# Kernel optimization log

Hardware: AMD Instinct MI355X
Metric: run time of the kernel (lower is better)

The kernel has to match this reference:

```python
import jax, jax.numpy as jnp
import numpy as np

N = 5000
E = 160000
H = 6   # num_heads
D = 64  # out feats per head
IN = 131


def _gat_layer(h, W, al, ar, b, src, dst, activate):
    """DGL-style GATConv: fc -> edge attention -> edge softmax -> scatter sum."""
    n = h.shape[0]
    f = (h @ W).reshape(n, H, D)                      # [N,H,D]
    el = (f * al).sum(-1)                             # [N,H]
    er = (f * ar).sum(-1)                             # [N,H]
    e = jax.nn.leaky_relu(el[src] + er[dst], 0.2)     # [E,H]
    emax = jax.ops.segment_max(e, dst, num_segments=n)
    ex = jnp.exp(e - emax[dst])
    den = jax.ops.segment_sum(ex, dst, num_segments=n)
    alpha = ex / den[dst]                             # [E,H] edge softmax per dst
    out = jax.ops.segment_sum(f[src] * alpha[:, :, None], dst, num_segments=n)
    out = out + b.reshape(H, D)
    return jax.nn.elu(out) if activate else out


def setup_inputs() -> dict:
    ks = jax.random.split(jax.random.key(0), 24)
    s = 0.05
    inp = {
        "nfeats": jax.random.normal(ks[0], (N, IN), jnp.float32),
        "dis": jax.random.uniform(ks[1], (N, N), jnp.float32),
        "src": jax.random.randint(ks[2], (E,), 0, N),
        "dst": jax.random.randint(ks[3], (E,), 0, N),
    }
    dims_in = [IN, H * D, H * D, H * D]
    for l in range(4):
        inp[f"w{l}"] = jax.random.normal(ks[4 + 4 * l], (dims_in[l], H * D), jnp.float32) * s
        inp[f"al{l}"] = jax.random.normal(ks[5 + 4 * l], (H, D), jnp.float32) * s
        inp[f"ar{l}"] = jax.random.normal(ks[6 + 4 * l], (H, D), jnp.float32) * s
        inp[f"b{l}"] = jax.random.normal(ks[7 + 4 * l], (H * D,), jnp.float32) * s
    inp["pw"] = jax.random.normal(ks[20], (129,), jnp.float32) * s
    inp["pb"] = jax.random.normal(ks[21], (), jnp.float32) * s
    return inp


def reference(nfeats, dis, src, dst,
              w0, al0, ar0, b0, w1, al1, ar1, b1,
              w2, al2, ar2, b2, w3, al3, ar3, b3, pw, pb):
    n = nfeats.shape[0]
    h = nfeats
    h = _gat_layer(h, w0, al0, ar0, b0, src, dst, True).reshape(n, H * D)
    h = _gat_layer(h, w1, al1, ar1, b1, src, dst, True).reshape(n, H * D)
    h = _gat_layer(h, w2, al2, ar2, b2, src, dst, True).reshape(n, H * D)
    emb = _gat_layer(h, w3, al3, ar3, b3, src, dst, False).mean(axis=1)  # [N,64]
    # pair_emb[i,j] = [emb[j], emb[i], dis[i,j]] -> Linear(129,1) -> tanh
    s1 = emb @ pw[:D]        # coefficient on emb[j]
    s2 = emb @ pw[D:2 * D]   # coefficient on emb[i]
    OD = jnp.tanh(s2[:, None] + s1[None, :] + dis * pw[2 * D] + pb)
    return OD
```

## Files before the change

kernel.cpp:

```cpp
#include <hip/hip_runtime.h>
#include <math.h>

#define N_NODES 5000
#define E_EDGES 160000
#define H_HEADS 6
#define D_FEAT  64
#define IN_FEAT 131
#define HD      384
#define NC4     (N_NODES/4)
#define AGG_CAP 1024
#define MPAD    5024
#define KP0     160

typedef float vf4   __attribute__((ext_vector_type(4)));
typedef float f32x4 __attribute__((ext_vector_type(4)));
typedef _Float16 h16;
typedef _Float16 half8 __attribute__((ext_vector_type(8)));

__global__ void k_count(const int* __restrict__ dst, int* __restrict__ deg) {
    int e = blockIdx.x * blockDim.x + threadIdx.x;
    if (e < E_EDGES) atomicAdd(&deg[dst[e]], 1);
}

__global__ void k_scan(int* __restrict__ deg, int* __restrict__ row_ptr) {
    __shared__ int part[1024];
    const int T = 1024;
    int t = threadIdx.x;
    const int per = (N_NODES + T - 1) / T;
    int start = t * per;
    int s = 0;
    for (int i = 0; i < per; i++) {
        int idx = start + i;
        if (idx < N_NODES) s += deg[idx];
    }
    part[t] = s;
    __syncthreads();
    for (int off = 1; off < T; off <<= 1) {
        int v = (t >= off) ? part[t - off] : 0;
        __syncthreads();
        part[t] += v;
        __syncthreads();
    }
    int excl = (t == 0) ? 0 : part[t - 1];
    for (int i = 0; i < per; i++) {
        int idx = start + i;
        if (idx < N_NODES) {
            row_ptr[idx] = excl;
            excl += deg[idx];
            deg[idx] = 0;
        }
    }
    if (t == T - 1) row_ptr[N_NODES] = part[T - 1];
}

__global__ void k_fill(const int* __restrict__ src, const int* __restrict__ dst,
                       const int* __restrict__ row_ptr,
                       int* __restrict__ cursor, int* __restrict__ csrc) {
    int e = blockIdx.x * blockDim.x + threadIdx.x;
    if (e < E_EDGES) {
        int d = dst[e];
        int p = atomicAdd(&cursor[d], 1);
        csrc[row_ptr[d] + p] = src[e];
    }
}

__global__ void k_cvt_a0(const float* __restrict__ A, h16* __restrict__ hi,
                         h16* __restrict__ lo) {
    int idx = blockIdx.x * blockDim.x + threadIdx.x;
    if (idx >= MPAD * KP0) return;
    int r = idx / KP0, k = idx - r * KP0;
    float v = (r < N_NODES && k < IN_FEAT) ? A[r * IN_FEAT + k] : 0.f;
    h16 h = (h16)v;
    hi[idx] = h;
    lo[idx] = (h16)(v - (float)h);
}

__global__ void k_cvt_w(const float* __restrict__ W, h16* __restrict__ hi,
                        h16* __restrict__ lo, int K, int KP) {
    int idx = blockIdx.x * blockDim.x + threadIdx.x;
    if (idx >= HD * KP) return;
    int n = idx / KP, k = idx - n * KP;
    float v = (k < K) ? W[(size_t)k * HD + n] : 0.f;
    h16 h = (h16)v;
    hi[idx] = h;
    lo[idx] = (h16)(v - (float)h);
}

__global__ __launch_bounds__(64, 2) void k_gemm_mfma(
        const h16* __restrict__ Ahi, const h16* __restrict__ Alo,
        const h16* __restrict__ Wthi, const h16* __restrict__ Wtlo,
        const float* __restrict__ al, const float* __restrict__ ar,
        float* __restrict__ C, float* __restrict__ el, float* __restrict__ er,
        int KP) {
    int lane = threadIdx.x;
    int h = blockIdx.x;
    int rb = blockIdx.y * 32;
    int cb = h * 64;
    int l15 = lane & 15, lg = lane >> 4;
    f32x4 acc[2][4] = {};

    const h16* a0h = Ahi + (size_t)(rb + l15) * KP + (lg << 3);
    const h16* a0l = Alo + (size_t)(rb + l15) * KP + (lg << 3);
    const h16* a1h = a0h + (size_t)16 * KP;
    const h16* a1l = a0l + (size_t)16 * KP;
    const h16* bh = Wthi + (size_t)(cb + l15) * KP + (lg << 3);
    const h16* bl = Wtlo + (size_t)(cb + l15) * KP + (lg << 3);

#pragma unroll 2
    for (int k0 = 0; k0 < KP; k0 += 32) {
        half8 A0h = *(const half8*)(a0h + k0);
        half8 A0l = *(const half8*)(a0l + k0);
        half8 A1h = *(const half8*)(a1h + k0);
        half8 A1l = *(const half8*)(a1l + k0);
#pragma unroll
        for (int t = 0; t < 4; t++) {
            half8 Bh = *(const half8*)(bh + (size_t)t * 16 * KP + k0);
            half8 Bl = *(const half8*)(bl + (size_t)t * 16 * KP + k0);
            acc[0][t] = __builtin_amdgcn_mfma_f32_16x16x32_f16(A0h, Bh, acc[0][t], 0, 0, 0);
            acc[0][t] = __builtin_amdgcn_mfma_f32_16x16x32_f16(A0l, Bh, acc[0][t], 0, 0, 0);
            acc[0][t] = __builtin_amdgcn_mfma_f32_16x16x32_f16(A0h, Bl, acc[0][t], 0, 0, 0);
            acc[1][t] = __builtin_amdgcn_mfma_f32_16x16x32_f16(A1h, Bh, acc[1][t], 0, 0, 0);
            acc[1][t] = __builtin_amdgcn_mfma_f32_16x16x32_f16(A1l, Bh, acc[1][t], 0, 0, 0);
            acc[1][t] = __builtin_amdgcn_mfma_f32_16x16x32_f16(A1h, Bl, acc[1][t], 0, 0, 0);
        }
    }

    float alv[4], arv[4];
#pragma unroll
    for (int t = 0; t < 4; t++) {
        alv[t] = al[h * D_FEAT + t * 16 + l15];
        arv[t] = ar[h * D_FEAT + t * 16 + l15];
    }
#pragma unroll
    for (int m = 0; m < 2; m++) {
#pragma unroll
        for (int r = 0; r < 4; r++) {
            int grow = rb + m * 16 + lg * 4 + r;
            float sl = 0.f, sr = 0.f;
#pragma unroll
            for (int t = 0; t < 4; t++) {
                float v = acc[m][t][r];
                if (grow < N_NODES) C[(size_t)grow * HD + cb + t * 16 + l15] = v;
                sl += v * alv[t];
                sr += v * arv[t];
            }
#pragma unroll
            for (int off = 1; off < 16; off <<= 1) {
                sl += __shfl_xor(sl, off);
                sr += __shfl_xor(sr, off);
            }
            if (l15 == 0 && grow < N_NODES) {
                el[grow * H_HEADS + h] = sl;
                er[grow * H_HEADS + h] = sr;
            }
        }
    }
}

__global__ __launch_bounds__(384) void k_agg(const float* __restrict__ f,
                                             const float* __restrict__ el,
                                             const float* __restrict__ er,
                                             const float* __restrict__ bias,
                                             const int* __restrict__ row_ptr,
                                             const int* __restrict__ csrc,
                                             float* __restrict__ out, int activate,
                                             h16* __restrict__ nhi,
                                             h16* __restrict__ nlo) {
    __shared__ int   s_src[AGG_CAP];
    __shared__ float s_x[H_HEADS][AGG_CAP];
    __shared__ float sh_inv[H_HEADS];
    int node = blockIdx.x;
    int t = threadIdx.x;
    int h = t >> 6, lane = t & 63;
    int r0 = row_ptr[node], r1 = row_ptr[node + 1];
    int deg = r1 - r0;
    int dcap = deg < AGG_CAP ? deg : AGG_CAP;
    float er_h = er[node * H_HEADS + h];

    for (int i = t; i < dcap; i += 384) s_src[i] = csrc[r0 + i];
    __syncthreads();

    float m = -1e30f;
    for (int i = lane; i < dcap; i += 64) {
        int s = s_src[i];
        float x = el[s * H_HEADS + h] + er_h;
        x = x >= 0.f ? x : 0.2f * x;
        s_x[h][i] = x;
        m = fmaxf(m, x);
    }
    for (int i = AGG_CAP + lane; i < deg; i += 64) {
        int s = csrc[r0 + i];
        float x = el[s * H_HEADS + h] + er_h;
        x = x >= 0.f ? x : 0.2f * x;
        m = fmaxf(m, x);
    }
    for (int off = 32; off; off >>= 1) m = fmaxf(m, __shfl_down(m, off));
    m = __shfl(m, 0);

    float ssum = 0.f;
    for (int i = lane; i < dcap; i += 64) {
        float w = __expf(s_x[h][i] - m);
        s_x[h][i] = w;
        ssum += w;
    }
    for (int i = AGG_CAP + lane; i < deg; i += 64) {
        int s = csrc[r0 + i];
        float x = el[s * H_HEADS + h] + er_h;
        x = x >= 0.f ? x : 0.2f * x;
        ssum += __expf(x - m);
    }
    for (int off = 32; off; off >>= 1) ssum += __shfl_down(ssum, off);
    if (lane == 0) sh_inv[h] = (ssum > 0.f) ? 1.f / ssum : 0.f;
    __syncthreads();
    float inv = sh_inv[h];

    const float* fh = f + h * D_FEAT + lane;
    float acc = 0.f;
    int i = 0;
    int lim = dcap & ~7;
    for (; i < lim; i += 8) {
        int s0 = s_src[i + 0], s1 = s_src[i + 1], s2 = s_src[i + 2], s3 = s_src[i + 3];
        int s4 = s_src[i + 4], s5 = s_src[i + 5], s6 = s_src[i + 6], s7 = s_src[i + 7];
        float f0 = fh[(size_t)s0 * HD], f1 = fh[(size_t)s1 * HD];
        float f2 = fh[(size_t)s2 * HD], f3 = fh[(size_t)s3 * HD];
        float f4 = fh[(size_t)s4 * HD], f5 = fh[(size_t)s5 * HD];
        float f6 = fh[(size_t)s6 * HD], f7 = fh[(size_t)s7 * HD];
        acc += s_x[h][i + 0] * f0;
        acc += s_x[h][i + 1] * f1;
        acc += s_x[h][i + 2] * f2;
        acc += s_x[h][i + 3] * f3;
        acc += s_x[h][i + 4] * f4;
        acc += s_x[h][i + 5] * f5;
        acc += s_x[h][i + 6] * f6;
        acc += s_x[h][i + 7] * f7;
    }
    for (; i < dcap; i++) {
        acc += s_x[h][i] * fh[(size_t)s_src[i] * HD];
    }
    for (i = AGG_CAP; i < deg; i++) {
        int s = csrc[r0 + i];
        float x = el[s * H_HEADS + h] + er_h;
        x = x >= 0.f ? x : 0.2f * x;
        acc += __expf(x - m) * fh[(size_t)s * HD];
    }
    float o = acc * inv + bias[h * D_FEAT + lane];
    if (activate) o = o > 0.f ? o : (__expf(o) - 1.f);
    int oi = node * HD + h * D_FEAT + lane;
    out[oi] = o;
    if (nhi) {
        h16 oh = (h16)o;
        nhi[oi] = oh;
        nlo[oi] = (h16)(o - (float)oh);
    }
}

__global__ void k_embed(const float* __restrict__ h3, const float* __restrict__ pw,
                        float* __restrict__ s1, float* __restrict__ s2) {
    int wave = (blockIdx.x * blockDim.x + threadIdx.x) >> 6;
    int lane = threadIdx.x & 63;
    if (wave >= N_NODES) return;
    float s = 0.f;
#pragma unroll
    for (int hh = 0; hh < H_HEADS; hh++) s += h3[wave * HD + hh * D_FEAT + lane];
    s *= (1.f / 6.f);
    float p1 = s * pw[lane];
    float p2 = s * pw[D_FEAT + lane];
    for (int off = 32; off; off >>= 1) {
        p1 += __shfl_down(p1, off);
        p2 += __shfl_down(p2, off);
    }
    if (lane == 0) { s1[wave] = p1; s2[wave] = p2; }
}

__device__ __forceinline__ float fast_tanh(float z) {
    float t = __expf(-2.f * fabsf(z));
    float r = (1.f - t) / (1.f + t);
    return copysignf(r, z);
}

__global__ void k_pair(const vf4* __restrict__ dis, const float* __restrict__ s1,
                       const float* __restrict__ s2, const float* __restrict__ pw,
                       const float* __restrict__ pb, vf4* __restrict__ out) {
    const int total = N_NODES * NC4;
    float w = pw[2 * D_FEAT];
    float b = pb[0];
    for (int idx = blockIdx.x * blockDim.x + threadIdx.x; idx < total;
         idx += gridDim.x * blockDim.x) {
        int i = idx / NC4;
        int j4 = idx - i * NC4;
        vf4 dv = __builtin_nontemporal_load(&dis[idx]);
        float base = s2[i] + b;
        int j = j4 * 4;
        vf4 o;
        o.x = fast_tanh(base + s1[j + 0] + dv.x * w);
        o.y = fast_tanh(base + s1[j + 1] + dv.y * w);
        o.z = fast_tanh(base + s1[j + 2] + dv.z * w);
        o.w = fast_tanh(base + s1[j + 3] + dv.w * w);
        __builtin_nontemporal_store(o, &out[idx]);
    }
}

extern "C" void kernel_launch(void* const* d_in, const int* in_sizes, int n_in,
                              void* d_out, int out_size, void* d_ws, size_t ws_size,
                              hipStream_t stream) {
    const float* nfeats = (const float*)d_in[0];
    const float* dis    = (const float*)d_in[1];
    const int*   src    = (const int*)d_in[2];
    const int*   dst    = (const int*)d_in[3];
    const float* w[4]  = {(const float*)d_in[4],  (const float*)d_in[8],
                          (const float*)d_in[12], (const float*)d_in[16]};
    const float* al[4] = {(const float*)d_in[5],  (const float*)d_in[9],
                          (const float*)d_in[13], (const float*)d_in[17]};
    const float* ar[4] = {(const float*)d_in[6],  (const float*)d_in[10],
                          (const float*)d_in[14], (const float*)d_in[18]};
    const float* bs[4] = {(const float*)d_in[7],  (const float*)d_in[11],
                          (const float*)d_in[15], (const float*)d_in[19]};
    const float* pw = (const float*)d_in[20];
    const float* pb = (const float*)d_in[21];
    float* out = (float*)d_out;

    float* f    = (float*)d_ws;
    float* hbuf = f + N_NODES * HD;
    float* el   = hbuf + N_NODES * HD;
    float* er   = el + N_NODES * H_HEADS;
    float* s1   = er + N_NODES * H_HEADS;
    float* s2   = s1 + N_NODES;
    int* row_ptr = (int*)(s2 + N_NODES);
    int* cursor  = row_ptr + (N_NODES + 1);
    int* csrc    = cursor + N_NODES;
    uintptr_t p = (uintptr_t)(csrc + E_EDGES);
    p = (p + 15) & ~(uintptr_t)15;
    h16* A0hi = (h16*)p;
    h16* A0lo = A0hi + (size_t)MPAD * KP0;
    h16* Athi = A0lo + (size_t)MPAD * KP0;
    h16* Atlo = Athi + (size_t)MPAD * HD;
    h16* Wthi = Atlo + (size_t)MPAD * HD;
    h16* Wtlo = Wthi + (size_t)HD * HD;

    (void)hipMemsetAsync(cursor, 0, N_NODES * sizeof(int), stream);
    k_count<<<(E_EDGES + 255) / 256, 256, 0, stream>>>(dst, cursor);
    k_scan<<<1, 1024, 0, stream>>>(cursor, row_ptr);
    k_fill<<<(E_EDGES + 255) / 256, 256, 0, stream>>>(src, dst, row_ptr, cursor, csrc);

    (void)hipMemsetAsync(Athi + (size_t)N_NODES * HD, 0,
                         (size_t)(MPAD - N_NODES) * HD * sizeof(h16), stream);
    (void)hipMemsetAsync(Atlo + (size_t)N_NODES * HD, 0,
                         (size_t)(MPAD - N_NODES) * HD * sizeof(h16), stream);

    dim3 gg(H_HEADS, (N_NODES + 31) / 32);

    k_cvt_a0<<<(MPAD * KP0 + 255) / 256, 256, 0, stream>>>(nfeats, A0hi, A0lo);
    k_cvt_w<<<(HD * KP0 + 255) / 256, 256, 0, stream>>>(w[0], Wthi, Wtlo, IN_FEAT, KP0);
    k_gemm_mfma<<<gg, 64, 0, stream>>>(A0hi, A0lo, Wthi, Wtlo, al[0], ar[0],
                                       f, el, er, KP0);
    k_agg<<<N_NODES, 384, 0, stream>>>(f, el, er, bs[0], row_ptr, csrc, hbuf, 1,
                                       Athi, Atlo);
    for (int l = 1; l < 4; l++) {
        k_cvt_w<<<(HD * HD + 255) / 256, 256, 0, stream>>>(w[l], Wthi, Wtlo, HD, HD);
        k_gemm_mfma<<<gg, 64, 0, stream>>>(Athi, Atlo, Wthi, Wtlo, al[l], ar[l],
                                           f, el, er, HD);
        k_agg<<<N_NODES, 384, 0, stream>>>(f, el, er, bs[l], row_ptr, csrc, hbuf,
                                           (l < 3) ? 1 : 0,
                                           (l < 3) ? Athi : (h16*)nullptr,
                                           (l < 3) ? Atlo : (h16*)nullptr);
    }
    k_embed<<<(N_NODES + 3) / 4, 256, 0, stream>>>(hbuf, pw, s1, s2);
    k_pair<<<4096, 256, 0, stream>>>((const vf4*)dis, s1, s2, pw, pb, (vf4*)out);
}
```

Measured before the change: 501.7 us.

## Fuse softmax into one pass with global max bound, batch weight conversions, fuse embed

The GEMM now records a per-head global max of el through an ordered-uint atomicMax. The aggregation kernel uses that bound, leaky-relu'd with each node's er, as the softmax shift, so it makes a single pass that computes the exp weights, weighted sum and denominator together, with no shared-memory score buffers or separate max pass. Weight conversion for all four layers runs in one tiled-transpose launch, the GEMM K loop is manually double-buffered in registers, and the final-layer mean and projection are folded into k_agg, dropping k_embed and the fp32 hbuf write. The risk is that the shift is an upper bound rather than the per-destination max, so large score gaps could underflow the exp weights, and the extra atomics and register pressure add cost.

```diff
diff --git a/kernel.cpp b/kernel.cpp
--- a/kernel.cpp
+++ b/kernel.cpp
@@ -17,6 +17,15 @@
 typedef _Float16 h16;
 typedef _Float16 half8 __attribute__((ext_vector_type(8)));
 
+__device__ __forceinline__ unsigned f2ord(float x) {
+    unsigned b = __float_as_uint(x);
+    return (b & 0x80000000u) ? ~b : (b | 0x80000000u);
+}
+__device__ __forceinline__ float ord2f(unsigned o) {
+    return (o & 0x80000000u) ? __uint_as_float(o & 0x7fffffffu)
+                             : __uint_as_float(~o);
+}
+
 __global__ void k_count(const int* __restrict__ dst, int* __restrict__ deg) {
     int e = blockIdx.x * blockDim.x + threadIdx.x;
     if (e < E_EDGES) atomicAdd(&deg[dst[e]], 1);
@@ -75,15 +84,72 @@
     lo[idx] = (h16)(v - (float)h);
 }
 
-__global__ void k_cvt_w(const float* __restrict__ W, h16* __restrict__ hi,
-                        h16* __restrict__ lo, int K, int KP) {
-    int idx = blockIdx.x * blockDim.x + threadIdx.x;
-    if (idx >= HD * KP) return;
-    int n = idx / KP, k = idx - n * KP;
-    float v = (k < K) ? W[(size_t)k * HD + n] : 0.f;
-    h16 h = (h16)v;
-    hi[idx] = h;
-    lo[idx] = (h16)(v - (float)h);
+struct CvtArgs {
+    const float *W0, *W1, *W2, *W3;
+    h16 *hi0, *lo0, *hi1, *lo1, *hi2, *lo2, *hi3, *lo3;
+};
+__global__ void k_cvt_wT(CvtArgs a) {
+    __shared__ float tile[32][33];
+    int z = blockIdx.z;
+    const float* W = z == 0 ? a.W0 : z == 1 ? a.W1 : z == 2 ? a.W2 : a.W3;
+    h16* hi = z == 0 ? a.hi0 : z == 1 ? a.hi1 : z == 2 ? a.hi2 : a.hi3;
+    h16* lo = z == 0 ? a.lo0 : z == 1 ? a.lo1 : z == 2 ? a.lo2 : a.lo3;
+    int K  = (z == 0) ? IN_FEAT : HD;
+    int KP = (z == 0) ? KP0 : HD;
+    int k0 = blockIdx.y * 32;
+    if (k0 >= KP) return;
+    int n0 = blockIdx.x * 32;
+    int tx = threadIdx.x & 31, ty = threadIdx.x >> 5;
+#pragma unroll
+    for (int j = 0; j < 4; j++) {
+        int kk = ty + j * 8;
+        int gk = k0 + kk;
+        tile[kk][tx] = (gk < K) ? W[(size_t)gk * HD + n0 + tx] : 0.f;
+    }
+    __syncthreads();
+#pragma unroll
+    for (int j = 0; j < 4; j++) {
+        int nn = ty + j * 8;
+        float v = tile[tx][nn];
+        h16 hh = (h16)v;
+        size_t o = (size_t)(n0 + nn) * KP + k0 + tx;
+        hi[o] = hh;
+        lo[o] = (h16)(v - (float)hh);
+    }
+}
+
+struct KRegs {
+    half8 a0h, a0l, a1h, a1l;
+    half8 bh0, bh1, bh2, bh3;
+    half8 bl0, bl1, bl2, bl3;
+};
+#define MF(A, B, C) C = __builtin_amdgcn_mfma_f32_16x16x32_f16(A, B, C, 0, 0, 0)
+
+__device__ __forceinline__ void load_step(KRegs& r,
+        const h16* a0h, const h16* a0l, const h16* a1h, const h16* a1l,
+        const h16* bh, const h16* bl, int KP, int k0) {
+    r.a0h = *(const half8*)(a0h + k0);
+    r.a0l = *(const half8*)(a0l + k0);
+    r.a1h = *(const half8*)(a1h + k0);
+    r.a1l = *(const half8*)(a1l + k0);
+    r.bh0 = *(const half8*)(bh + k0);
+    r.bh1 = *(const half8*)(bh + (size_t)16 * KP + k0);
+    r.bh2 = *(const half8*)(bh + (size_t)32 * KP + k0);
+    r.bh3 = *(const half8*)(bh + (size_t)48 * KP + k0);
+    r.bl0 = *(const half8*)(bl + k0);
+    r.bl1 = *(const half8*)(bl + (size_t)16 * KP + k0);
+    r.bl2 = *(const half8*)(bl + (size_t)32 * KP + k0);
+    r.bl3 = *(const half8*)(bl + (size_t)48 * KP + k0);
+}
+__device__ __forceinline__ void mfma_step(const KRegs& r, f32x4 acc[2][4]) {
+    MF(r.a0h, r.bh0, acc[0][0]); MF(r.a0l, r.bh0, acc[0][0]); MF(r.a0h, r.bl0, acc[0][0]);
+    MF(r.a1h, r.bh0, acc[1][0]); MF(r.a1l, r.bh0, acc[1][0]); MF(r.a1h, r.bl0, acc[1][0]);
+    MF(r.a0h, r.bh1, acc[0][1]); MF(r.a0l, r.bh1, acc[0][1]); MF(r.a0h, r.bl1, acc[0][1]);
+    MF(r.a1h, r.bh1, acc[1][1]); MF(r.a1l, r.bh1, acc[1][1]); MF(r.a1h, r.bl1, acc[1][1]);
+    MF(r.a0h, r.bh2, acc[0][2]); MF(r.a0l, r.bh2, acc[0][2]); MF(r.a0h, r.bl2, acc[0][2]);
+    MF(r.a1h, r.bh2, acc[1][2]); MF(r.a1l, r.bh2, acc[1][2]); MF(r.a1h, r.bl2, acc[1][2]);
+    MF(r.a0h, r.bh3, acc[0][3]); MF(r.a0l, r.bh3, acc[0][3]); MF(r.a0h, r.bl3, acc[0][3]);
+    MF(r.a1h, r.bh3, acc[1][3]); MF(r.a1l, r.bh3, acc[1][3]); MF(r.a1h, r.bl3, acc[1][3]);
 }
 
 __global__ __launch_bounds__(64, 2) void k_gemm_mfma(
@@ -91,7 +157,7 @@
         const h16* __restrict__ Wthi, const h16* __restrict__ Wtlo,
         const float* __restrict__ al, const float* __restrict__ ar,
         float* __restrict__ C, float* __restrict__ el, float* __restrict__ er,
-        int KP) {
+        unsigned* __restrict__ maxel, int KP) {
     int lane = threadIdx.x;
     int h = blockIdx.x;
     int rb = blockIdx.y * 32;
@@ -106,31 +172,26 @@
     const h16* bh = Wthi + (size_t)(cb + l15) * KP + (lg << 3);
     const h16* bl = Wtlo + (size_t)(cb + l15) * KP + (lg << 3);
 
-#pragma unroll 2
-    for (int k0 = 0; k0 < KP; k0 += 32) {
-        half8 A0h = *(const half8*)(a0h + k0);
-        half8 A0l = *(const half8*)(a0l + k0);
-        half8 A1h = *(const half8*)(a1h + k0);
-        half8 A1l = *(const half8*)(a1l + k0);
-#pragma unroll
-        for (int t = 0; t < 4; t++) {
-            half8 Bh = *(const half8*)(bh + (size_t)t * 16 * KP + k0);
-            half8 Bl = *(const half8*)(bl + (size_t)t * 16 * KP + k0);
-            acc[0][t] = __builtin_amdgcn_mfma_f32_16x16x32_f16(A0h, Bh, acc[0][t], 0, 0, 0);
-            acc[0][t] = __builtin_amdgcn_mfma_f32_16x16x32_f16(A0l, Bh, acc[0][t], 0, 0, 0);
-            acc[0][t] = __builtin_amdgcn_mfma_f32_16x16x32_f16(A0h, Bl, acc[0][t], 0, 0, 0);
-            acc[1][t] = __builtin_amdgcn_mfma_f32_16x16x32_f16(A1h, Bh, acc[1][t], 0, 0, 0);
-            acc[1][t] = __builtin_amdgcn_mfma_f32_16x16x32_f16(A1l, Bh, acc[1][t], 0, 0, 0);
-            acc[1][t] = __builtin_amdgcn_mfma_f32_16x16x32_f16(A1h, Bl, acc[1][t], 0, 0, 0);
-        }
-    }
+    KRegs r0, r1;
+    load_step(r0, a0h, a0l, a1h, a1l, bh, bl, KP, 0);
+    const int T = KP >> 5;
+    int t = 0;
+    for (; t + 2 <= T; t += 2) {
+        load_step(r1, a0h, a0l, a1h, a1l, bh, bl, KP, (t + 1) << 5);
+        mfma_step(r0, acc);
+        if (t + 2 < T)
+            load_step(r0, a0h, a0l, a1h, a1l, bh, bl, KP, (t + 2) << 5);
+        mfma_step(r1, acc);
+    }
+    if (t < T) mfma_step(r0, acc);
 
     float alv[4], arv[4];
 #pragma unroll
-    for (int t = 0; t < 4; t++) {
-        alv[t] = al[h * D_FEAT + t * 16 + l15];
-        arv[t] = ar[h * D_FEAT + t * 16 + l15];
-    }
+    for (int q = 0; q < 4; q++) {
+        alv[q] = al[h * D_FEAT + q * 16 + l15];
+        arv[q] = ar[h * D_FEAT + q * 16 + l15];
+    }
+    float elmax = -1e30f;
 #pragma unroll
     for (int m = 0; m < 2; m++) {
 #pragma unroll
@@ -138,138 +199,112 @@
             int grow = rb + m * 16 + lg * 4 + r;
             float sl = 0.f, sr = 0.f;
 #pragma unroll
-            for (int t = 0; t < 4; t++) {
-                float v = acc[m][t][r];
-                if (grow < N_NODES) C[(size_t)grow * HD + cb + t * 16 + l15] = v;
-                sl += v * alv[t];
-                sr += v * arv[t];
+            for (int q = 0; q < 4; q++) {
+                float v = acc[m][q][r];
+                if (grow < N_NODES) C[(size_t)grow * HD + cb + q * 16 + l15] = v;
+                sl += v * alv[q];
+                sr += v * arv[q];
             }
 #pragma unroll
             for (int off = 1; off < 16; off <<= 1) {
                 sl += __shfl_xor(sl, off);
                 sr += __shfl_xor(sr, off);
             }
+            elmax = fmaxf(elmax, sl);
             if (l15 == 0 && grow < N_NODES) {
                 el[grow * H_HEADS + h] = sl;
                 er[grow * H_HEADS + h] = sr;
             }
         }
     }
-}
-
-__global__ __launch_bounds__(384) void k_agg(const float* __restrict__ f,
-                                             const float* __restrict__ el,
-                                             const float* __restrict__ er,
-                                             const float* __restrict__ bias,
-                                             const int* __restrict__ row_ptr,
-                                             const int* __restrict__ csrc,
-                                             float* __restrict__ out, int activate,
-                                             h16* __restrict__ nhi,
-                                             h16* __restrict__ nlo) {
+    elmax = fmaxf(elmax, __shfl_xor(elmax, 16));
+    elmax = fmaxf(elmax, __shfl_xor(elmax, 32));
+    if (lane == 0) atomicMax(&maxel[h], f2ord(elmax));
+}
+
+__global__ __launch_bounds__(384) void k_agg(
+        const float* __restrict__ f, const float* __restrict__ el,
+        const float* __restrict__ er, const float* __restrict__ bias,
+        const int* __restrict__ row_ptr, const int* __restrict__ csrc,
+        const unsigned* __restrict__ maxel,
+        h16* __restrict__ nhi, h16* __restrict__ nlo,
+        const float* __restrict__ pw,
+        float* __restrict__ s1g, float* __restrict__ s2g, int last) {
     __shared__ int   s_src[AGG_CAP];
-    __shared__ float s_x[H_HEADS][AGG_CAP];
-    __shared__ float sh_inv[H_HEADS];
+    __shared__ float s_o[H_HEADS][D_FEAT];
     int node = blockIdx.x;
     int t = threadIdx.x;
     int h = t >> 6, lane = t & 63;
-    int r0 = row_ptr[node], r1 = row_ptr[node + 1];
-    int deg = r1 - r0;
+    int r0 = row_ptr[node], deg = row_ptr[node + 1] - r0;
     int dcap = deg < AGG_CAP ? deg : AGG_CAP;
     float er_h = er[node * H_HEADS + h];
+    float M = ord2f(maxel[h]) + er_h;
+    M = M >= 0.f ? M : 0.2f * M;
 
     for (int i = t; i < dcap; i += 384) s_src[i] = csrc[r0 + i];
     __syncthreads();
 
-    float m = -1e30f;
-    for (int i = lane; i < dcap; i += 64) {
+    const float* fh = f + h * D_FEAT + lane;
+    float acc = 0.f, ssum = 0.f;
+    int i = 0;
+    int lim = dcap & ~3;
+    for (; i < lim; i += 4) {
+        int sA = s_src[i + 0], sB = s_src[i + 1];
+        int sC = s_src[i + 2], sD = s_src[i + 3];
+        float eA = el[sA * H_HEADS + h], eB = el[sB * H_HEADS + h];
+        float eC = el[sC * H_HEADS + h], eD = el[sD * H_HEADS + h];
+        float gA = fh[(size_t)sA * HD], gB = fh[(size_t)sB * HD];
+        float gC = fh[(size_t)sC * HD], gD = fh[(size_t)sD * HD];
+        float x;
+        x = eA + er_h; x = x >= 0.f ? x : 0.2f * x; float wA = __expf(x - M);
+        x = eB + er_h; x = x >= 0.f ? x : 0.2f * x; float wB = __expf(x - M);
+        x = eC + er_h; x = x >= 0.f ? x : 0.2f * x; float wC = __expf(x - M);
+        x = eD + er_h; x = x >= 0.f ? x : 0.2f * x; float wD = __expf(x - M);
+        acc += wA * gA; acc += wB * gB; acc += wC * gC; acc += wD * gD;
+        ssum += wA + wB + wC + wD;
+    }
+    for (; i < dcap; i++) {
         int s = s_src[i];
-        float x = el[s * H_HEADS + h] + er_h;
-        x = x >= 0.f ? x : 0.2f * x;
-        s_x[h][i] = x;
-        m = fmaxf(m, x);
-    }
-    for (int i = AGG_CAP + lane; i < deg; i += 64) {
-        int s = csrc[r0 + i];
-        float x = el[s * H_HEADS + h] + er_h;
-        x = x >= 0.f ? x : 0.2f * x;
-        m = fmaxf(m, x);
-    }
-    for (int off = 32; off; off >>= 1) m = fmaxf(m, __shfl_down(m, off));
-    m = __shfl(m, 0);
-
-    float ssum = 0.f;
-    for (int i = lane; i < dcap; i += 64) {
-        float w = __expf(s_x[h][i] - m);
-        s_x[h][i] = w;
-        ssum += w;
-    }
-    for (int i = AGG_CAP + lane; i < deg; i += 64) {
-        int s = csrc[r0 + i];
-        float x = el[s * H_HEADS + h] + er_h;
-        x = x >= 0.f ? x : 0.2f * x;
-        ssum += __expf(x - m);
-    }
-    for (int off = 32; off; off >>= 1) ssum += __shfl_down(ssum, off);
-    if (lane == 0) sh_inv[h] = (ssum > 0.f) ? 1.f / ssum : 0.f;
-    __syncthreads();
-    float inv = sh_inv[h];
-
-    const float* fh = f + h * D_FEAT + lane;
-    float acc = 0.f;
-    int i = 0;
-    int lim = dcap & ~7;
-    for (; i < lim; i += 8) {
-        int s0 = s_src[i + 0], s1 = s_src[i + 1], s2 = s_src[i + 2], s3 = s_src[i + 3];
-        int s4 = s_src[i + 4], s5 = s_src[i + 5], s6 = s_src[i + 6], s7 = s_src[i + 7];
-        float f0 = fh[(size_t)s0 * HD], f1 = fh[(size_t)s1 * HD];
-        float f2 = fh[(size_t)s2 * HD], f3 = fh[(size_t)s3 * HD];
-        float f4 = fh[(size_t)s4 * HD], f5 = fh[(size_t)s5 * HD];
-        float f6 = fh[(size_t)s6 * HD], f7 = fh[(size_t)s7 * HD];
-        acc += s_x[h][i + 0] * f0;
-        acc += s_x[h][i + 1] * f1;
-        acc += s_x[h][i + 2] * f2;
-        acc += s_x[h][i + 3] * f3;
-        acc += s_x[h][i + 4] * f4;
-        acc += s_x[h][i + 5] * f5;
-        acc += s_x[h][i + 6] * f6;
-        acc += s_x[h][i + 7] * f7;
-    }
-    for (; i < dcap; i++) {
-        acc += s_x[h][i] * fh[(size_t)s_src[i] * HD];
-    }
-    for (i = AGG_CAP; i < deg; i++) {
-        int s = csrc[r0 + i];
-        float x = el[s * H_HEADS + h] + er_h;
-        x = x >= 0.f ? x : 0.2f * x;
-        acc += __expf(x - m) * fh[(size_t)s * HD];
-    }
+        float e = el[s * H_HEADS + h];
+        float g = fh[(size_t)s * HD];
+        float x = e + er_h; x = x >= 0.f ? x : 0.2f * x;
+        float w = __expf(x - M);
+        acc += w * g; ssum += w;
+    }
+    for (int i2 = AGG_CAP; i2 < deg; i2++) {
+        int s = csrc[r0 + i2];
+        float e = el[s * H_HEADS + h];
+        float g = fh[(size_t)s * HD];
+        float x = e + er_h; x = x >= 0.f ? x : 0.2f * x;
+        float w = __expf(x - M);
+        acc += w * g; ssum += w;
+    }
+    float inv = ssum > 0.f ? 1.f / ssum : 0.f;
     float o = acc * inv + bias[h * D_FEAT + lane];
-    if (activate) o = o > 0.f ? o : (__expf(o) - 1.f);
-    int oi = node * HD + h * D_FEAT + lane;
-    out[oi] = o;
-    if (nhi) {
-        h16 oh = (h16)o;
+
+    if (!last) {
+        float oa = o > 0.f ? o : (__expf(o) - 1.f);
+        int oi = node * HD + h * D_FEAT + lane;
+        h16 oh = (h16)oa;
         nhi[oi] = oh;
-        nlo[oi] = (h16)(o - (float)oh);
-    }
-}
-
-__global__ void k_embed(const float* __restrict__ h3, const float* __restrict__ pw,
-                        float* __restrict__ s1, float* __restrict__ s2) {
-    int wave = (blockIdx.x * blockDim.x + threadIdx.x) >> 6;
-    int lane = threadIdx.x & 63;
-    if (wave >= N_NODES) return;
-    float s = 0.f;
-#pragma unroll
-    for (int hh = 0; hh < H_HEADS; hh++) s += h3[wave * HD + hh * D_FEAT + lane];
-    s *= (1.f / 6.f);
-    float p1 = s * pw[lane];
-    float p2 = s * pw[D_FEAT + lane];
-    for (int off = 32; off; off >>= 1) {
-        p1 += __shfl_down(p1, off);
-        p2 += __shfl_down(p2, off);
-    }
-    if (lane == 0) { s1[wave] = p1; s2[wave] = p2; }
+        nlo[oi] = (h16)(oa - (float)oh);
+    } else {
+        s_o[h][lane] = o;
+        __syncthreads();
+        if (t < 64) {
+            float s = 0.f;
+#pragma unroll
+            for (int hh = 0; hh < H_HEADS; hh++) s += s_o[hh][t];
+            s *= (1.f / 6.f);
+            float p1 = s * pw[t];
+            float p2 = s * pw[D_FEAT + t];
+            for (int off = 32; off; off >>= 1) {
+                p1 += __shfl_down(p1, off);
+                p2 += __shfl_down(p2, off);
+            }
+            if (t == 0) { s1g[node] = p1; s2g[node] = p2; }
+        }
+    }
 }
 
 __device__ __forceinline__ float fast_tanh(float z) {
@@ -319,25 +354,32 @@
     const float* pb = (const float*)d_in[21];
     float* out = (float*)d_out;
 
-    float* f    = (float*)d_ws;
-    float* hbuf = f + N_NODES * HD;
-    float* el   = hbuf + N_NODES * HD;
-    float* er   = el + N_NODES * H_HEADS;
-    float* s1   = er + N_NODES * H_HEADS;
-    float* s2   = s1 + N_NODES;
+    float* f     = (float*)d_ws;
+    float* el    = f + (size_t)N_NODES * HD;
+    float* er    = el + N_NODES * H_HEADS;
+    float* s1    = er + N_NODES * H_HEADS;
+    float* s2    = s1 + N_NODES;
     int* row_ptr = (int*)(s2 + N_NODES);
     int* cursor  = row_ptr + (N_NODES + 1);
     int* csrc    = cursor + N_NODES;
-    uintptr_t p = (uintptr_t)(csrc + E_EDGES);
+    unsigned* maxel = (unsigned*)(csrc + E_EDGES);
+    uintptr_t p = (uintptr_t)(maxel + 32);
     p = (p + 15) & ~(uintptr_t)15;
     h16* A0hi = (h16*)p;
     h16* A0lo = A0hi + (size_t)MPAD * KP0;
     h16* Athi = A0lo + (size_t)MPAD * KP0;
     h16* Atlo = Athi + (size_t)MPAD * HD;
-    h16* Wthi = Atlo + (size_t)MPAD * HD;
-    h16* Wtlo = Wthi + (size_t)HD * HD;
+    h16* Wt0hi = Atlo + (size_t)MPAD * HD;
+    h16* Wt0lo = Wt0hi + (size_t)HD * KP0;
+    h16* Wt1hi = Wt0lo + (size_t)HD * KP0;
+    h16* Wt1lo = Wt1hi + (size_t)HD * HD;
+    h16* Wt2hi = Wt1lo + (size_t)HD * HD;
+    h16* Wt2lo = Wt2hi + (size_t)HD * HD;
+    h16* Wt3hi = Wt2lo + (size_t)HD * HD;
+    h16* Wt3lo = Wt3hi + (size_t)HD * HD;
 
     (void)hipMemsetAsync(cursor, 0, N_NODES * sizeof(int), stream);
+    (void)hipMemsetAsync(maxel, 0, 32 * sizeof(unsigned), stream);
     k_count<<<(E_EDGES + 255) / 256, 256, 0, stream>>>(dst, cursor);
     k_scan<<<1, 1024, 0, stream>>>(cursor, row_ptr);
     k_fill<<<(E_EDGES + 255) / 256, 256, 0, stream>>>(src, dst, row_ptr, cursor, csrc);
@@ -347,23 +389,26 @@
     (void)hipMemsetAsync(Atlo + (size_t)N_NODES * HD, 0,
                          (size_t)(MPAD - N_NODES) * HD * sizeof(h16), stream);
 
+    k_cvt_a0<<<(MPAD * KP0 + 255) / 256, 256, 0, stream>>>(nfeats, A0hi, A0lo);
+    CvtArgs ca = {w[0], w[1], w[2], w[3],
+                  Wt0hi, Wt0lo, Wt1hi, Wt1lo, Wt2hi, Wt2lo, Wt3hi, Wt3lo};
+    k_cvt_wT<<<dim3(HD / 32, HD / 32, 4), 256, 0, stream>>>(ca);
+
     dim3 gg(H_HEADS, (N_NODES + 31) / 32);
-
-    k_cvt_a0<<<(MPAD * KP0 + 255) / 256, 256, 0, stream>>>(nfeats, A0hi, A0lo);
-    k_cvt_w<<<(HD * KP0 + 255) / 256, 256, 0, stream>>>(w[0], Wthi, Wtlo, IN_FEAT, KP0);
-    k_gemm_mfma<<<gg, 64, 0, stream>>>(A0hi, A0lo, Wthi, Wtlo, al[0], ar[0],
-                                       f, el, er, KP0);
-    k_agg<<<N_NODES, 384, 0, stream>>>(f, el, er, bs[0], row_ptr, csrc, hbuf, 1,
-                                       Athi, Atlo);
-    for (int l = 1; l < 4; l++) {
-        k_cvt_w<<<(HD * HD + 255) / 256, 256, 0, stream>>>(w[l], Wthi, Wtlo, HD, HD);
-        k_gemm_mfma<<<gg, 64, 0, stream>>>(Athi, Atlo, Wthi, Wtlo, al[l], ar[l],
-                                           f, el, er, HD);
-        k_agg<<<N_NODES, 384, 0, stream>>>(f, el, er, bs[l], row_ptr, csrc, hbuf,
-                                           (l < 3) ? 1 : 0,
-                                           (l < 3) ? Athi : (h16*)nullptr,
-                                           (l < 3) ? Atlo : (h16*)nullptr);
-    }
-    k_embed<<<(N_NODES + 3) / 4, 256, 0, stream>>>(hbuf, pw, s1, s2);
+    const h16* Whi[4] = {Wt0hi, Wt1hi, Wt2hi, Wt3hi};
+    const h16* Wlo[4] = {Wt0lo, Wt1lo, Wt2lo, Wt3lo};
+    for (int l = 0; l < 4; l++) {
+        const h16* Ahi = (l == 0) ? A0hi : Athi;
+        const h16* Alo = (l == 0) ? A0lo : Atlo;
+        int KP = (l == 0) ? KP0 : HD;
+        k_gemm_mfma<<<gg, 64, 0, stream>>>(Ahi, Alo, Whi[l], Wlo[l], al[l], ar[l],
+                                           f, el, er, maxel + l * 8, KP);
+        int last = (l == 3);
+        k_agg<<<N_NODES, 384, 0, stream>>>(f, el, er, bs[l], row_ptr, csrc,
+                                           maxel + l * 8,
+                                           last ? (h16*)nullptr : Athi,
+                                           last ? (h16*)nullptr : Atlo,
+                                           pw, s1, s2, last);
+    }
     k_pair<<<4096, 256, 0, stream>>>((const vf4*)dis, s1, s2, pw, pb, (vf4*)out);
 }
```

Measured after the change: 525.0 us. +4.7%, slower.
